# Kernel tuning notes

Measured on AMD Instinct MI355X. Metric: run time of the kernel, lower is better.

Reference implementation:

```python
import jax, jax.numpy as jnp
import numpy as np

B, S, D = 8, 4096, 256


def setup_inputs() -> dict:
    key = jax.random.key(0)
    kq, kk, kv, kb = jax.random.split(key, 4)
    q = jax.random.normal(kq, (B, S, D), dtype=jnp.float32)
    k = jax.random.normal(kk, (B, S, D), dtype=jnp.float32)
    v = jax.random.normal(kv, (B, S, D), dtype=jnp.float32)
    beta = jax.random.uniform(kb, (B, S), dtype=jnp.float32)
    return {"q": q, "k": k, "v": v, "beta": beta}


def reference(q, k, v, beta):
    # Delta-rule linear attention recurrence:
    #   h_t = beta_t * h_{t-1} + k_t^T v_t   (h: [B, D, D])
    #   o_t = q_t @ h_t                      (o: [B, D])
    dtype = q.dtype
    b, s, d = q.shape
    h0 = jnp.zeros((b, d, d), dtype=dtype)

    def step(h, inp):
        q_t, k_t, v_t, b_t = inp  # q_t/k_t/v_t: [B, D], b_t: [B]
        h = h * b_t[:, None, None] + jnp.einsum('bi,bj->bij', k_t, v_t)
        o_t = jnp.einsum('bi,bij->bj', q_t, h)
        return h, o_t

    xs = (q.transpose(1, 0, 2), k.transpose(1, 0, 2),
          v.transpose(1, 0, 2), beta.T)  # time-major
    _, out = jax.lax.scan(step, h0, xs)  # out: [S, B, D]
    return out.transpose(1, 0, 2)  # [B, S, D]
```

## Files before the change

kernel.cpp:

```cpp
#include <hip/hip_runtime.h>
#include <hip/hip_bf16.h>
#include <math.h>


#define B_ 8
#define S_ 4096
#define D_ 256
#define L_ 128
#define C_ (S_ / L_)
#define BC_ (B_ * C_)
#define STK 66

typedef __attribute__((ext_vector_type(8))) short s8v;
typedef __attribute__((ext_vector_type(4))) float f4v;
typedef unsigned short u16;
typedef unsigned int u32;

__device__ __forceinline__ u32 pk2(float lo, float hi) {
  union { __hip_bfloat162 h; u32 u; } cv;
  cv.h = __float22bfloat162_rn(make_float2(lo, hi));
  return cv.u;
}
__device__ __forceinline__ s8v pack8(const float4 a, const float4 b) {
  union { u32 u[4]; s8v v; } r;
  r.u[0] = pk2(a.x, a.y); r.u[1] = pk2(a.z, a.w);
  r.u[2] = pk2(b.x, b.y); r.u[3] = pk2(b.z, b.w);
  return r.v;
}

__device__ __forceinline__ void beta_scan128(const float* betap, float* ls,
                                             int tid) {
  if (tid < 64) {
    float x = log2f(fmaxf(betap[tid], 1e-30f));
#pragma unroll
    for (int off = 1; off < 64; off <<= 1) {
      float y = __shfl_up(x, off);
      if (tid >= off) x += y;
    }
    ls[tid] = x;
    const float tot0 = __shfl(x, 63);
    float z = log2f(fmaxf(betap[64 + tid], 1e-30f));
#pragma unroll
    for (int off = 1; off < 64; off <<= 1) {
      float y = __shfl_up(z, off);
      if (tid >= off) z += y;
    }
    ls[64 + tid] = z + tot0;
  }
}

__global__ __launch_bounds__(512, 2) void ks_summary5(
    const float* __restrict__ kg, const float* __restrict__ vg,
    const float* __restrict__ beta, u16* __restrict__ A,
    float* __restrict__ P)
{
  __shared__ float ls[L_];
  __shared__ __align__(16) u16 U[2][256 * STK];
  __shared__ __align__(16) u16 BN[64 * 264];

  const int bc = blockIdx.x;
  const int b = bc / C_, c = bc % C_;
  const int tid = threadIdx.x;
  const float* betap = beta + (size_t)b * S_ + (size_t)c * L_;
  const float* kbase = kg + ((size_t)b * S_ + (size_t)c * L_) * D_;
  const float* vbase = vg + ((size_t)b * S_ + (size_t)c * L_) * D_;

  beta_scan128(betap, ls, tid);
  __syncthreads();
  const float ltot = ls[L_ - 1];
  if (tid == 0) P[bc] = exp2f(ltot);

  const int hh = tid >> 8;
  const int t2 = tid & 255;
  const int iLs = t2 & 7;
  const int s0s = (t2 >> 3) * 2;
  const int sg = hh * 64 + s0s;

  {
    const float* src0 = kbase + (size_t)sg * D_;
    const float* src1 = src0 + D_;
    const float w0 = exp2f(ltot - ls[sg]);
    const float w1 = exp2f(ltot - ls[sg + 1]);
    u16* dst = U[hh];
#pragma unroll
    for (int p = 0; p < 8; ++p) {
      const int i0 = p * 32 + iLs * 4;
      float a0[4], a1[4];
      *(float4*)a0 = *(const float4*)(src0 + i0);
      *(float4*)a1 = *(const float4*)(src1 + i0);
#pragma unroll
      for (int u = 0; u < 4; ++u)
        *(u32*)&dst[(i0 + u) * STK + s0s] = pk2(a0[u] * w0, a1[u] * w1);
    }
  }
  __syncthreads();

  const int lane = tid & 63, wave = tid >> 6;
  const int quad = lane >> 4, l15 = lane & 15;
  const int i0w = wave * 32;

  s8v af[2][4];
#pragma unroll
  for (int mt = 0; mt < 2; ++mt)
#pragma unroll
    for (int ks = 0; ks < 4; ++ks)
      af[mt][ks] = *(const s8v*)&U[ks >> 1][(i0w + mt * 16 + l15) * STK +
                                            (ks & 1) * 32 + quad * 8];
  __syncthreads();

  {
    const float* src0 = vbase + (size_t)sg * D_;
    const float* src1 = src0 + D_;
    u16* dst = U[hh];
#pragma unroll
    for (int p = 0; p < 8; ++p) {
      const int i0 = p * 32 + iLs * 4;
      float a0[4], a1[4];
      *(float4*)a0 = *(const float4*)(src0 + i0);
      *(float4*)a1 = *(const float4*)(src1 + i0);
#pragma unroll
      for (int u = 0; u < 4; ++u)
        *(u32*)&dst[(i0 + u) * STK + s0s] = pk2(a0[u], a1[u]);
    }
  }
  __syncthreads();

  u16* Ab = A + (size_t)bc * D_ * D_;

  for (int ng = 0; ng < 4; ++ng) {
    f4v acc[2][4];
#pragma unroll
    for (int mt = 0; mt < 2; ++mt)
#pragma unroll
      for (int nt = 0; nt < 4; ++nt) acc[mt][nt] = (f4v){0.f, 0.f, 0.f, 0.f};

#pragma unroll
    for (int ks = 0; ks < 4; ++ks) {
      const int so = (ks & 1) * 32 + quad * 8;
      s8v bv[4];
#pragma unroll
      for (int nt = 0; nt < 4; ++nt)
        bv[nt] = *(const s8v*)&U[ks >> 1][(ng * 64 + nt * 16 + l15) * STK + so];
#pragma unroll
      for (int mt = 0; mt < 2; ++mt)
#pragma unroll
        for (int nt = 0; nt < 4; ++nt)
          acc[mt][nt] = __builtin_amdgcn_mfma_f32_16x16x32_bf16(
              af[mt][ks], bv[nt], acc[mt][nt], 0, 0, 0);
    }
#pragma unroll
    for (int mt = 0; mt < 2; ++mt)
#pragma unroll
      for (int nt = 0; nt < 4; ++nt) {
        const int jl = nt * 16 + l15;
        uint2 w;
        w.x = pk2(acc[mt][nt][0], acc[mt][nt][1]);
        w.y = pk2(acc[mt][nt][2], acc[mt][nt][3]);
        *(uint2*)&BN[jl * 264 + i0w + mt * 16 + quad * 4] = w;
      }
    __syncthreads();
    {
      const int jl = tid >> 3;
      const int il = (tid & 7) * 8;
#pragma unroll
      for (int p = 0; p < 4; ++p) {
        const int iu = il + p * 64;
        *(s8v*)&Ab[(size_t)(ng * 64 + jl) * D_ + iu] =
            *(const s8v*)&BN[jl * 264 + iu];
      }
    }
    __syncthreads();
  }
}

__global__ __launch_bounds__(256) void ks_scan5(
    u16* __restrict__ A, const float* __restrict__ P)
{
  const int g = blockIdx.x;
  const int b = g >> 7;
  const int idx = ((g & 127) << 8) + threadIdx.x;
  u16* base = A + (size_t)b * ((size_t)C_ * D_ * D_) + (size_t)idx * 2;
  const float* Pb = P + b * C_;

  float h0 = 0.f, h1 = 0.f;
  u32 cur = *(const u32*)base;
  u32 nx = *(const u32*)(base + (size_t)(D_ * D_));
  float pc = Pb[0], pn = Pb[1];
#pragma unroll 4
  for (int c = 0; c < C_; ++c) {
    u16* p = base + (size_t)c * (D_ * D_);
    u32 n2 = 0; float p2 = 0.f;
    if (c + 2 < C_) {
      n2 = *(const u32*)(p + 2 * (size_t)(D_ * D_));
      p2 = Pb[c + 2];
    }
    const float a0 = __uint_as_float(cur << 16);
    const float a1 = __uint_as_float(cur & 0xFFFF0000u);
    *(u32*)p = pk2(h0, h1);
    h0 = fmaf(pc, h0, a0);
    h1 = fmaf(pc, h1, a1);
    cur = nx; pc = pn; nx = n2; pn = p2;
  }
}

__global__ __launch_bounds__(512, 2) void ks_output5(
    const float* __restrict__ qg, const float* __restrict__ kg,
    const float* __restrict__ vg, const float* __restrict__ beta,
    const u16* __restrict__ Hg, float* __restrict__ outg)
{
  __shared__ float ls[L_];
  __shared__ float cv[L_];
  __shared__ __align__(16) u16 QB[L_ * 264];
  __shared__ __align__(16) u16 Tm[L_ * 136];
  __shared__ __align__(16) u16 VT[256 * STK];

  const int bc = blockIdx.x;
  const int b = bc / C_, c = bc % C_;
  const int tid = threadIdx.x;
  const float* betap = beta + (size_t)b * S_ + (size_t)c * L_;
  const float* qbase = qg + ((size_t)b * S_ + (size_t)c * L_) * D_;
  const float* kbase = kg + ((size_t)b * S_ + (size_t)c * L_) * D_;
  const float* vbase = vg + ((size_t)b * S_ + (size_t)c * L_) * D_;
  const u16* Hb = Hg + (size_t)bc * D_ * D_;

  beta_scan128(betap, ls, tid);

  {
    const int t = tid >> 2;
    const int cg = (tid & 3) * 8;
    const float* src = qbase + (size_t)t * D_ + cg;
#pragma unroll
    for (int p = 0; p < 8; ++p) {
      const s8v pk = pack8(*(const float4*)(src + p * 32),
                           *(const float4*)(src + p * 32 + 4));
      *(s8v*)&QB[t * 264 + cg + p * 32] = pk;
    }
  }
  __syncthreads();
  if (tid < L_) cv[tid] = exp2f(ls[tid]);

  const int lane = tid & 63, wave = tid >> 6;
  const int quad = lane >> 4, l15 = lane & 15;

  {
    const int mA = wave * 16;
    f4v accA[8];
#pragma unroll
    for (int i = 0; i < 8; ++i) accA[i] = (f4v){0.f, 0.f, 0.f, 0.f};
#pragma unroll
    for (int kd = 0; kd < 8; ++kd) {
      const int d0 = kd * 32 + quad * 8;
      const float* krow = kbase + (size_t)(mA + l15) * D_ + d0;
      const s8v af = pack8(*(const float4*)krow, *(const float4*)(krow + 4));
#pragma unroll
      for (int nt = 0; nt < 8; ++nt) {
        const s8v bf = *(const s8v*)&QB[(nt * 16 + l15) * 264 + d0];
        accA[nt] = __builtin_amdgcn_mfma_f32_16x16x32_bf16(af, bf, accA[nt],
                                                           0, 0, 0);
      }
    }
#pragma unroll
    for (int nt = 0; nt < 8; ++nt) {
      const int t = nt * 16 + l15;
      const float lt = ls[t];
      const int s0 = mA + quad * 4;
      float v[4];
#pragma unroll
      for (int r = 0; r < 4; ++r) {
        const int s = s0 + r;
        v[r] = (s <= t) ? accA[nt][r] * exp2f(lt - ls[s]) : 0.f;
      }
      uint2 w;
      w.x = pk2(v[0], v[1]);
      w.y = pk2(v[2], v[3]);
      *(uint2*)&Tm[t * 136 + s0] = w;
    }
  }
  __syncthreads();

  const int j0w = wave * 32;
  f4v acc[2][8];
#pragma unroll
  for (int mt = 0; mt < 2; ++mt)
#pragma unroll
    for (int nt = 0; nt < 8; ++nt) acc[mt][nt] = (f4v){0.f, 0.f, 0.f, 0.f};

#pragma unroll
  for (int ks = 0; ks < 8; ++ks) {
    const int io = ks * 32 + quad * 8;
    s8v af[2], bf[8];
#pragma unroll
    for (int mt = 0; mt < 2; ++mt)
      af[mt] = *(const s8v*)(Hb + (size_t)(j0w + mt * 16 + l15) * D_ + io);
#pragma unroll
    for (int nt = 0; nt < 8; ++nt)
      bf[nt] = *(const s8v*)&QB[(nt * 16 + l15) * 264 + io];
#pragma unroll
    for (int mt = 0; mt < 2; ++mt)
#pragma unroll
      for (int nt = 0; nt < 8; ++nt)
        acc[mt][nt] = __builtin_amdgcn_mfma_f32_16x16x32_bf16(
            af[mt], bf[nt], acc[mt][nt], 0, 0, 0);
  }
#pragma unroll
  for (int nt = 0; nt < 8; ++nt) {
    const float ct = cv[nt * 16 + l15];
#pragma unroll
    for (int mt = 0; mt < 2; ++mt) {
      acc[mt][nt][0] *= ct; acc[mt][nt][1] *= ct;
      acc[mt][nt][2] *= ct; acc[mt][nt][3] *= ct;
    }
  }

#pragma unroll
  for (int h = 0; h < 2; ++h) {
    __syncthreads();
    {
      const int iL = tid & 15;
      const int s0 = ((tid >> 4) & 31) * 2;
      const float* src0 = vbase + (size_t)(h * 64 + s0) * D_;
      const float* src1 = src0 + D_;
#pragma unroll
      for (int p = 0; p < 4; ++p) {
        const int i0 = p * 64 + iL * 4;
        float a0[4], a1[4];
        *(float4*)a0 = *(const float4*)(src0 + i0);
        *(float4*)a1 = *(const float4*)(src1 + i0);
#pragma unroll
        for (int u = 0; u < 4; ++u)
          *(u32*)&VT[(i0 + u) * STK + s0] = pk2(a0[u], a1[u]);
      }
    }
    __syncthreads();
#pragma unroll
    for (int ks = 0; ks < 2; ++ks) {
      const int so = ks * 32 + quad * 8;
      s8v af[2], bf[8];
#pragma unroll
      for (int mt = 0; mt < 2; ++mt)
        af[mt] = *(const s8v*)&VT[(j0w + mt * 16 + l15) * STK + so];
#pragma unroll
      for (int nt = 0; nt < 8; ++nt)
        bf[nt] = *(const s8v*)&Tm[(nt * 16 + l15) * 136 + h * 64 + so];
#pragma unroll
      for (int mt = 0; mt < 2; ++mt)
#pragma unroll
        for (int nt = 0; nt < 8; ++nt)
          acc[mt][nt] = __builtin_amdgcn_mfma_f32_16x16x32_bf16(
              af[mt], bf[nt], acc[mt][nt], 0, 0, 0);
    }
  }

  float* ob = outg + ((size_t)b * S_ + (size_t)c * L_) * D_;
#pragma unroll
  for (int mt = 0; mt < 2; ++mt)
#pragma unroll
    for (int nt = 0; nt < 8; ++nt) {
      const int t = nt * 16 + l15;
      const int j0 = j0w + mt * 16 + quad * 4;
      float4 o;
      o.x = acc[mt][nt][0]; o.y = acc[mt][nt][1];
      o.z = acc[mt][nt][2]; o.w = acc[mt][nt][3];
      *(float4*)(ob + (size_t)t * D_ + j0) = o;
    }
}

extern "C" void kernel_launch(void* const* d_in, const int* in_sizes, int n_in,
                              void* d_out, int out_size, void* d_ws,
                              size_t ws_size, hipStream_t stream) {
  const float* q = (const float*)d_in[0];
  const float* k = (const float*)d_in[1];
  const float* v = (const float*)d_in[2];
  const float* beta = (const float*)d_in[3];
  float* out = (float*)d_out;

  u16* A = (u16*)d_ws;
  float* P = (float*)((char*)d_ws + (size_t)BC_ * D_ * D_ * sizeof(u16));

  ks_summary5<<<dim3(BC_), dim3(512), 0, stream>>>(k, v, beta, A, P);
  ks_scan5<<<dim3(1024), dim3(256), 0, stream>>>(A, P);
  ks_output5<<<dim3(BC_), dim3(512), 0, stream>>>(q, k, v, beta, A, out);
}
```

Before: 175.5 us.

## Batch-load chunk states in scan and overlap V/H loads in output kernel

The scan kernel now has each thread handle four state elements and issue all 32 chunk loads up front into registers, then do the recurrence and write everything back. This replaces the old rolling two-deep prefetch and halves the grid. The output kernel moves the first V-transpose staging ahead of the first barrier, software-pipelines the global H fragment loads across the k-loop, and drops one synchronization phase. Costs are higher register pressure (64 uint values per scan thread) and fewer scan blocks to hide latency.

```diff
diff --git a/kernel.cpp b/kernel.cpp
--- a/kernel.cpp
+++ b/kernel.cpp
@@ -49,7 +49,7 @@
   }
 }
 
-__global__ __launch_bounds__(512, 2) void ks_summary5(
+__global__ __launch_bounds__(512, 2) void ks_summary6(
     const float* __restrict__ kg, const float* __restrict__ vg,
     const float* __restrict__ beta, u16* __restrict__ A,
     float* __restrict__ P)
@@ -173,37 +173,40 @@
   }
 }
 
-__global__ __launch_bounds__(256) void ks_scan5(
+__global__ __launch_bounds__(256) void ks_scan6(
     u16* __restrict__ A, const float* __restrict__ P)
 {
   const int g = blockIdx.x;
-  const int b = g >> 7;
-  const int idx = ((g & 127) << 8) + threadIdx.x;
-  u16* base = A + (size_t)b * ((size_t)C_ * D_ * D_) + (size_t)idx * 2;
+  const int b = g >> 6;
+  const int unit = ((g & 63) << 8) + threadIdx.x;
+  u16* base = A + (size_t)b * ((size_t)C_ * D_ * D_) + (size_t)unit * 4;
   const float* Pb = P + b * C_;
 
-  float h0 = 0.f, h1 = 0.f;
-  u32 cur = *(const u32*)base;
-  u32 nx = *(const u32*)(base + (size_t)(D_ * D_));
-  float pc = Pb[0], pn = Pb[1];
-#pragma unroll 4
+  uint2 d[C_];
+#pragma unroll
+  for (int c = 0; c < C_; ++c)
+    d[c] = *(const uint2*)(base + (size_t)c * (D_ * D_));
+
+  float h0 = 0.f, h1 = 0.f, h2 = 0.f, h3 = 0.f;
+#pragma unroll
   for (int c = 0; c < C_; ++c) {
-    u16* p = base + (size_t)c * (D_ * D_);
-    u32 n2 = 0; float p2 = 0.f;
-    if (c + 2 < C_) {
-      n2 = *(const u32*)(p + 2 * (size_t)(D_ * D_));
-      p2 = Pb[c + 2];
-    }
-    const float a0 = __uint_as_float(cur << 16);
-    const float a1 = __uint_as_float(cur & 0xFFFF0000u);
-    *(u32*)p = pk2(h0, h1);
-    h0 = fmaf(pc, h0, a0);
-    h1 = fmaf(pc, h1, a1);
-    cur = nx; pc = pn; nx = n2; pn = p2;
-  }
-}
-
-__global__ __launch_bounds__(512, 2) void ks_output5(
+    const float pc = Pb[c];
+    const uint2 u = d[c];
+    const float a0 = __uint_as_float(u.x << 16);
+    const float a1 = __uint_as_float(u.x & 0xFFFF0000u);
+    const float a2 = __uint_as_float(u.y << 16);
+    const float a3 = __uint_as_float(u.y & 0xFFFF0000u);
+    d[c].x = pk2(h0, h1);
+    d[c].y = pk2(h2, h3);
+    h0 = fmaf(pc, h0, a0); h1 = fmaf(pc, h1, a1);
+    h2 = fmaf(pc, h2, a2); h3 = fmaf(pc, h3, a3);
+  }
+#pragma unroll
+  for (int c = 0; c < C_; ++c)
+    *(uint2*)(base + (size_t)c * (D_ * D_)) = d[c];
+}
+
+__global__ __launch_bounds__(512, 2) void ks_output6(
     const float* __restrict__ qg, const float* __restrict__ kg,
     const float* __restrict__ vg, const float* __restrict__ beta,
     const u16* __restrict__ Hg, float* __restrict__ outg)
@@ -241,6 +244,7 @@
 
   const int lane = tid & 63, wave = tid >> 6;
   const int quad = lane >> 4, l15 = lane & 15;
+  const int j0w = wave * 32;
 
   {
     const int mA = wave * 16;
@@ -276,9 +280,31 @@
       *(uint2*)&Tm[t * 136 + s0] = w;
     }
   }
-  __syncthreads();
-
-  const int j0w = wave * 32;
+
+  {
+    const int iL = tid & 15;
+    const int s0 = ((tid >> 4) & 31) * 2;
+    const float* src0 = vbase + (size_t)s0 * D_;
+    const float* src1 = src0 + D_;
+#pragma unroll
+    for (int p = 0; p < 4; ++p) {
+      const int i0 = p * 64 + iL * 4;
+      float a0[4], a1[4];
+      *(float4*)a0 = *(const float4*)(src0 + i0);
+      *(float4*)a1 = *(const float4*)(src1 + i0);
+#pragma unroll
+      for (int u = 0; u < 4; ++u)
+        *(u32*)&VT[(i0 + u) * STK + s0] = pk2(a0[u], a1[u]);
+    }
+  }
+
+  s8v hc[2];
+#pragma unroll
+  for (int mt = 0; mt < 2; ++mt)
+    hc[mt] = *(const s8v*)(Hb + (size_t)(j0w + mt * 16 + l15) * D_ + quad * 8);
+
+  __syncthreads();
+
   f4v acc[2][8];
 #pragma unroll
   for (int mt = 0; mt < 2; ++mt)
@@ -288,13 +314,45 @@
 #pragma unroll
   for (int ks = 0; ks < 8; ++ks) {
     const int io = ks * 32 + quad * 8;
-    s8v af[2], bf[8];
-#pragma unroll
-    for (int mt = 0; mt < 2; ++mt)
-      af[mt] = *(const s8v*)(Hb + (size_t)(j0w + mt * 16 + l15) * D_ + io);
+    s8v hn[2] = {hc[0], hc[1]};
+    if (ks < 7) {
+#pragma unroll
+      for (int mt = 0; mt < 2; ++mt)
+        hn[mt] = *(const s8v*)(Hb + (size_t)(j0w + mt * 16 + l15) * D_ +
+                               io + 32);
+    }
+    s8v bf[8];
 #pragma unroll
     for (int nt = 0; nt < 8; ++nt)
       bf[nt] = *(const s8v*)&QB[(nt * 16 + l15) * 264 + io];
+#pragma unroll
+    for (int mt = 0; mt < 2; ++mt)
+#pragma unroll
+      for (int nt = 0; nt < 8; ++nt)
+        acc[mt][nt] = __builtin_amdgcn_mfma_f32_16x16x32_bf16(
+            hc[mt], bf[nt], acc[mt][nt], 0, 0, 0);
+    hc[0] = hn[0]; hc[1] = hn[1];
+  }
+#pragma unroll
+  for (int nt = 0; nt < 8; ++nt) {
+    const float ct = cv[nt * 16 + l15];
+#pragma unroll
+    for (int mt = 0; mt < 2; ++mt) {
+      acc[mt][nt][0] *= ct; acc[mt][nt][1] *= ct;
+      acc[mt][nt][2] *= ct; acc[mt][nt][3] *= ct;
+    }
+  }
+
+#pragma unroll
+  for (int ks = 0; ks < 2; ++ks) {
+    const int so = ks * 32 + quad * 8;
+    s8v af[2], bf[8];
+#pragma unroll
+    for (int mt = 0; mt < 2; ++mt)
+      af[mt] = *(const s8v*)&VT[(j0w + mt * 16 + l15) * STK + so];
+#pragma unroll
+    for (int nt = 0; nt < 8; ++nt)
+      bf[nt] = *(const s8v*)&Tm[(nt * 16 + l15) * 136 + so];
 #pragma unroll
     for (int mt = 0; mt < 2; ++mt)
 #pragma unroll
@@ -302,53 +360,41 @@
         acc[mt][nt] = __builtin_amdgcn_mfma_f32_16x16x32_bf16(
             af[mt], bf[nt], acc[mt][nt], 0, 0, 0);
   }
-#pragma unroll
-  for (int nt = 0; nt < 8; ++nt) {
-    const float ct = cv[nt * 16 + l15];
-#pragma unroll
-    for (int mt = 0; mt < 2; ++mt) {
-      acc[mt][nt][0] *= ct; acc[mt][nt][1] *= ct;
-      acc[mt][nt][2] *= ct; acc[mt][nt][3] *= ct;
-    }
-  }
-
-#pragma unroll
-  for (int h = 0; h < 2; ++h) {
-    __syncthreads();
-    {
-      const int iL = tid & 15;
-      const int s0 = ((tid >> 4) & 31) * 2;
-      const float* src0 = vbase + (size_t)(h * 64 + s0) * D_;
-      const float* src1 = src0 + D_;
-#pragma unroll
-      for (int p = 0; p < 4; ++p) {
-        const int i0 = p * 64 + iL * 4;
-        float a0[4], a1[4];
-        *(float4*)a0 = *(const float4*)(src0 + i0);
-        *(float4*)a1 = *(const float4*)(src1 + i0);
-#pragma unroll
-        for (int u = 0; u < 4; ++u)
-          *(u32*)&VT[(i0 + u) * STK + s0] = pk2(a0[u], a1[u]);
-      }
-    }
-    __syncthreads();
-#pragma unroll
-    for (int ks = 0; ks < 2; ++ks) {
-      const int so = ks * 32 + quad * 8;
-      s8v af[2], bf[8];
-#pragma unroll
-      for (int mt = 0; mt < 2; ++mt)
-        af[mt] = *(const s8v*)&VT[(j0w + mt * 16 + l15) * STK + so];
+
+  __syncthreads();
+  {
+    const int iL = tid & 15;
+    const int s0 = ((tid >> 4) & 31) * 2;
+    const float* src0 = vbase + (size_t)(64 + s0) * D_;
+    const float* src1 = src0 + D_;
+#pragma unroll
+    for (int p = 0; p < 4; ++p) {
+      const int i0 = p * 64 + iL * 4;
+      float a0[4], a1[4];
+      *(float4*)a0 = *(const float4*)(src0 + i0);
+      *(float4*)a1 = *(const float4*)(src1 + i0);
+#pragma unroll
+      for (int u = 0; u < 4; ++u)
+        *(u32*)&VT[(i0 + u) * STK + s0] = pk2(a0[u], a1[u]);
+    }
+  }
+  __syncthreads();
+#pragma unroll
+  for (int ks = 0; ks < 2; ++ks) {
+    const int so = ks * 32 + quad * 8;
+    s8v af[2], bf[8];
+#pragma unroll
+    for (int mt = 0; mt < 2; ++mt)
+      af[mt] = *(const s8v*)&VT[(j0w + mt * 16 + l15) * STK + so];
+#pragma unroll
+    for (int nt = 0; nt < 8; ++nt)
+      bf[nt] = *(const s8v*)&Tm[(nt * 16 + l15) * 136 + 64 + so];
+#pragma unroll
+    for (int mt = 0; mt < 2; ++mt)
 #pragma unroll
       for (int nt = 0; nt < 8; ++nt)
-        bf[nt] = *(const s8v*)&Tm[(nt * 16 + l15) * 136 + h * 64 + so];
-#pragma unroll
-      for (int mt = 0; mt < 2; ++mt)
-#pragma unroll
-        for (int nt = 0; nt < 8; ++nt)
-          acc[mt][nt] = __builtin_amdgcn_mfma_f32_16x16x32_bf16(
-              af[mt], bf[nt], acc[mt][nt], 0, 0, 0);
-    }
+        acc[mt][nt] = __builtin_amdgcn_mfma_f32_16x16x32_bf16(
+            af[mt], bf[nt], acc[mt][nt], 0, 0, 0);
   }
 
   float* ob = outg + ((size_t)b * S_ + (size_t)c * L_) * D_;
@@ -377,7 +423,7 @@
   u16* A = (u16*)d_ws;
   float* P = (float*)((char*)d_ws + (size_t)BC_ * D_ * D_ * sizeof(u16));
 
-  ks_summary5<<<dim3(BC_), dim3(512), 0, stream>>>(k, v, beta, A, P);
-  ks_scan5<<<dim3(1024), dim3(256), 0, stream>>>(A, P);
-  ks_output5<<<dim3(BC_), dim3(512), 0, stream>>>(q, k, v, beta, A, out);
-}
+  ks_summary6<<<dim3(BC_), dim3(512), 0, stream>>>(k, v, beta, A, P);
+  ks_scan6<<<dim3(512), dim3(256), 0, stream>>>(A, P);
+  ks_output6<<<dim3(BC_), dim3(512), 0, stream>>>(q, k, v, beta, A, out);
+}
```

Result: faster. 172.0 us (-2.0%).
